# Kernel tuning notes

Measured on AMD Instinct MI355X. Metric: run time of the kernel, lower is better.

## Reference

```python
import jax, jax.numpy as jnp
import numpy as np

NUM_CAPS = 8
IN_CH = 768
OUT_CH = 64  # == num_routes
BATCH = 16384


def setup_inputs() -> dict:
    key = jax.random.key(0)
    ks = jax.random.split(key, 9)
    lim = 1.0 / np.sqrt(IN_CH)  # torch Linear default init range
    inp = {
        'img_emb': jax.random.normal(ks[0], (BATCH, IN_CH), jnp.float32),
        'capt_emb': jax.random.normal(ks[1], (BATCH, IN_CH), jnp.float32),
        'dct_emb': jax.random.normal(ks[2], (BATCH, IN_CH), jnp.float32),
        'W_img': jax.random.uniform(ks[3], (NUM_CAPS, OUT_CH, IN_CH), jnp.float32, -lim, lim),
        'b_img': jax.random.uniform(ks[4], (NUM_CAPS, OUT_CH), jnp.float32, -lim, lim),
        'W_capt': jax.random.uniform(ks[5], (NUM_CAPS, OUT_CH, IN_CH), jnp.float32, -lim, lim),
        'b_capt': jax.random.uniform(ks[6], (NUM_CAPS, OUT_CH), jnp.float32, -lim, lim),
        'W_dct': jax.random.uniform(ks[7], (NUM_CAPS, OUT_CH, IN_CH), jnp.float32, -lim, lim),
        'b_dct': jax.random.uniform(ks[8], (NUM_CAPS, OUT_CH), jnp.float32, -lim, lim),
    }
    return inp


def _project(x, W, b):
    # x: [B, I]; W: [C, R, I]; b: [C, R] -> [B, R, C]
    # torch: per-capsule Linear y = x @ W_c.T + b_c, viewed [B, R, 1], cat on last dim
    y = jnp.einsum('bi,cri->brc', x, W) + b.T[None]  # [B, R, C]
    return y


def _squash(u, epsilon=1e-07):
    sq = jnp.sum(u * u, axis=-1, keepdims=True)  # [B, 3R, 1]
    safe_norm = jnp.sqrt(sq + epsilon)
    return sq * u / ((1.0 + sq) * safe_norm)


def reference(img_emb, capt_emb, dct_emb, W_img, b_img, W_capt, b_capt, W_dct, b_dct):
    u_img = _project(img_emb, W_img, b_img)      # [B, 64, 8]
    u_capt = _project(capt_emb, W_capt, b_capt)  # [B, 64, 8]
    u_dct = _project(dct_emb, W_dct, b_dct)      # [B, 64, 8]
    combined = jnp.concatenate([u_img, u_capt, u_dct], axis=1)  # [B, 192, 8]
    return _squash(combined)
```

## Files before the change

### kernel.cpp

```cpp
#include <hip/hip_runtime.h>

typedef __attribute__((ext_vector_type(8))) short short8;
typedef __attribute__((ext_vector_type(4))) float floatx4;
typedef __attribute__((ext_vector_type(4))) unsigned int uintx4;

#if __has_builtin(__builtin_amdgcn_cvt_pk_bf16_f32)
typedef __attribute__((ext_vector_type(2))) __bf16 bf16x2;
__device__ __forceinline__ unsigned int pk_bf16(float a, float b) {
  bf16x2 v = __builtin_amdgcn_cvt_pk_bf16_f32(a, b);
  return __builtin_bit_cast(unsigned int, v);
}
#else
__device__ __forceinline__ unsigned int bf16_1(float f) {
  unsigned int u = __builtin_bit_cast(unsigned int, f);
  return (u + 0x7fffu + ((u >> 16) & 1u)) >> 16;
}
__device__ __forceinline__ unsigned int pk_bf16(float a, float b) {
  return bf16_1(a) | (bf16_1(b) << 16);
}
#endif


__global__ __launch_bounds__(256) void prep_w(
    const float* __restrict__ Wi, const float* __restrict__ Wc, const float* __restrict__ Wd,
    const float* __restrict__ bi, const float* __restrict__ bc, const float* __restrict__ bd,
    uintx4* __restrict__ Bprep, float* __restrict__ biasPrep) {
  const int t = blockIdx.x * 256 + threadIdx.x;
  const int l = t & 63;
  const int frag = t >> 6;
  const int nt = frag & 3;
  const int q = frag >> 2;
  const int ks = q % 24;
  const int q2 = q / 24;
  const int h = q2 & 7;
  const int mod = q2 >> 3;
  const int n16 = h * 4 + nt;
  const float* __restrict__ W = (mod == 0) ? Wi : ((mod == 1) ? Wc : Wd);

  const int n = n16 * 16 + (l & 15);
  const int r = n >> 3;
  const int c = n & 7;
  const int i0 = ks * 32 + (l >> 4) * 8;
  const float* src = W + (size_t)(c * 64 + r) * 768 + i0;
  floatx4 f0 = *(const floatx4*)(src);
  floatx4 f1 = *(const floatx4*)(src + 4);
  uintx4 p;
  p.x = pk_bf16(f0.x, f0.y);
  p.y = pk_bf16(f0.z, f0.w);
  p.z = pk_bf16(f1.x, f1.y);
  p.w = pk_bf16(f1.z, f1.w);
  Bprep[(size_t)frag * 64 + l] = p;

  if (t < 1536) {
    const int m2 = t >> 9;
    const int nn = t & 511;
    const float* bb = (m2 == 0) ? bi : ((m2 == 1) ? bc : bd);
    biasPrep[t] = bb[(nn & 7) * 64 + (nn >> 3)];
  }
}

#define LOADA(aa, kk)                                                        \
  {                                                                          \
    _Pragma("unroll") for (int mt = 0; mt < 2; ++mt)                         \
        aa[mt] = Afr[((kk) * 2 + mt) * 64 +                                  \
                     ((ln ^ (((kk) * 4 + quad) & 15)) + (quad << 4))];       \
  }

#define LOADB(bb, kk)                                                        \
  {                                                                          \
    _Pragma("unroll") for (int n2 = 0; n2 < 4; ++n2)                         \
        bb[n2] = bbase[((kk) * 4 + n2) * 64];                                \
  }

#define COMP(aa, bb)                                                     \
  {                                                                      \
    _Pragma("unroll") for (int mt = 0; mt < 2; ++mt)                     \
    {                                                                    \
      short8 af = __builtin_bit_cast(short8, aa[mt]);                    \
      _Pragma("unroll") for (int n2 = 0; n2 < 4; ++n2)                   \
          acc[mt][n2] = __builtin_amdgcn_mfma_f32_16x16x32_bf16(         \
              af, __builtin_bit_cast(short8, bb[n2]), acc[mt][n2], 0, 0, \
              0);                                                        \
    }                                                                    \
  }

__global__ __launch_bounds__(512, 4) void caps_fused(
    const float* __restrict__ x0, const float* __restrict__ x1, const float* __restrict__ x2,
    const uintx4* __restrict__ Bprep, const float* __restrict__ biasPrep,
    float* __restrict__ out) {
  __shared__ unsigned long long As64[48 * 128];

  const int tid = threadIdx.x;
  const int bx0 = blockIdx.x;
  const int bx = (bx0 & 7) * 192 + (bx0 >> 3);
  const int mod = bx >> 9;
  const int bm = bx & 511;
  const float* __restrict__ X = (mod == 0) ? x0 : ((mod == 1) ? x1 : x2);

  const float* src = X + (size_t)bm * 32 * 768;
#pragma unroll
  for (int i = 0; i < 12; ++i) {
    const int idx = i * 2048 + tid * 4;
    floatx4 f = __builtin_nontemporal_load((const floatx4*)(src + idx));
    const int m = (unsigned)idx / 768u;
    const int k = idx - m * 768;
    const int ks = k >> 5;
    const int kk = k & 31;
    const int qk = kk >> 3;
    const int jh = (kk >> 2) & 1;
    const int mt = m >> 4;
    const int lnn = m & 15;
    const int p = (ks * 4 + qk) & 15;
    const int slot = (lnn ^ p) + (qk << 4);
    unsigned long long w =
        ((unsigned long long)pk_bf16(f.z, f.w) << 32) | pk_bf16(f.x, f.y);
    As64[(((ks * 2 + mt) * 64 + slot) << 1) + jh] = w;
  }
  __syncthreads();

  const int lane = tid & 63;
  const int ln = lane & 15;
  const int quad = lane >> 4;
  const int wv = tid >> 6;

  const uintx4* Afr = (const uintx4*)As64;
  const uintx4* bbase = Bprep + (size_t)(mod * 8 + wv) * (96 * 64) + lane;

  floatx4 acc[2][4] = {};
  uintx4 a0[2], a1[2], a2[2], b0[4], b1[4], b2[4];

  LOADA(a0, 0); LOADB(b0, 0);
  LOADA(a1, 1); LOADB(b1, 1);
  LOADA(a2, 2); LOADB(b2, 2);
#pragma unroll
  for (int it = 0; it < 7; ++it) {
    const int s = 3 * it;
    COMP(a0, b0);
    LOADA(a0, s + 3); LOADB(b0, s + 3);
    COMP(a1, b1);
    LOADA(a1, s + 4); LOADB(b1, s + 4);
    COMP(a2, b2);
    LOADA(a2, s + 5); LOADB(b2, s + 5);
  }
  COMP(a0, b0);
  COMP(a1, b1);
  COMP(a2, b2);

  const int col0 = mod * 512 + wv * 64 + ln;
  float bias[4];
#pragma unroll
  for (int n2 = 0; n2 < 4; ++n2) bias[n2] = biasPrep[col0 + n2 * 16];

#pragma unroll
  for (int mt = 0; mt < 2; ++mt) {
    float* opm = out + (size_t)(bm * 32 + mt * 16 + quad * 4) * 1536 + col0;
#pragma unroll
    for (int jj = 0; jj < 4; ++jj) {
      float* opj = opm + jj * 1536;
#pragma unroll
      for (int n2 = 0; n2 < 4; ++n2) {
        float u = acc[mt][n2][jj] + bias[n2];
        float s = u * u;
        s += __shfl_xor(s, 1);
        s += __shfl_xor(s, 2);
        s += __shfl_xor(s, 4);
#if __has_builtin(__builtin_amdgcn_rsqf) && __has_builtin(__builtin_amdgcn_rcpf)
        float sc = s * __builtin_amdgcn_rsqf(s + 1e-7f) *
                   __builtin_amdgcn_rcpf(1.0f + s);
#else
        float sc = s / ((1.0f + s) * sqrtf(s + 1e-7f));
#endif
        opj[n2 * 16] = u * sc;
      }
    }
  }
}

extern "C" void kernel_launch(void* const* d_in, const int* in_sizes, int n_in,
                              void* d_out, int out_size, void* d_ws, size_t ws_size,
                              hipStream_t stream) {
  const float* ximg = (const float*)d_in[0];
  const float* xcapt = (const float*)d_in[1];
  const float* xdct = (const float*)d_in[2];
  const float* Wi = (const float*)d_in[3];
  const float* bi = (const float*)d_in[4];
  const float* Wc = (const float*)d_in[5];
  const float* bc = (const float*)d_in[6];
  const float* Wd = (const float*)d_in[7];
  const float* bd = (const float*)d_in[8];

  uintx4* Bprep = (uintx4*)d_ws;
  float* biasPrep = (float*)((char*)d_ws + 2304 * 1024);

  hipLaunchKernelGGL(prep_w, dim3(576), dim3(256), 0, stream,
                     Wi, Wc, Wd, bi, bc, bd, Bprep, biasPrep);
  hipLaunchKernelGGL(caps_fused, dim3(1536), dim3(512), 0, stream,
                     ximg, xcapt, xdct, (const uintx4*)Bprep, biasPrep,
                     (float*)d_out);
}
```

Before: 92.79 us.

## Make caps kernel persistent with register-resident weight fragments per half-strip

The fused kernel becomes persistent with 510 blocks. Each block handles one modality and one half of the 512 output columns and loops over row tiles with a stride of 85. Each wave loads its 48 bf16 B fragments into registers once, so the per-tile weight reloads from global or L2 go away. The cost is that every A tile is now staged and converted twice, once per column half. The design also needs heavy register use (launch bounds drop to 2 blocks), loses the nontemporal loads, and has no overlap between the A-tile load and compute within a block.

```diff
diff --git a/kernel.cpp b/kernel.cpp
--- a/kernel.cpp
+++ b/kernel.cpp
@@ -66,111 +66,117 @@
                      ((ln ^ (((kk) * 4 + quad) & 15)) + (quad << 4))];       \
   }
 
-#define LOADB(bb, kk)                                                        \
-  {                                                                          \
-    _Pragma("unroll") for (int n2 = 0; n2 < 4; ++n2)                         \
-        bb[n2] = bbase[((kk) * 4 + n2) * 64];                                \
-  }
-
-#define COMP(aa, bb)                                                     \
+#define COMP(aa, kk)                                                     \
   {                                                                      \
     _Pragma("unroll") for (int mt = 0; mt < 2; ++mt)                     \
     {                                                                    \
       short8 af = __builtin_bit_cast(short8, aa[mt]);                    \
-      _Pragma("unroll") for (int n2 = 0; n2 < 4; ++n2)                   \
+      _Pragma("unroll") for (int n2 = 0; n2 < 2; ++n2)                   \
           acc[mt][n2] = __builtin_amdgcn_mfma_f32_16x16x32_bf16(         \
-              af, __builtin_bit_cast(short8, bb[n2]), acc[mt][n2], 0, 0, \
-              0);                                                        \
+              af, __builtin_bit_cast(short8, Bfr[(kk) * 2 + n2]),        \
+              acc[mt][n2], 0, 0, 0);                                     \
     }                                                                    \
   }
 
-__global__ __launch_bounds__(512, 4) void caps_fused(
+__global__ __launch_bounds__(512, 2) void caps_fused(
     const float* __restrict__ x0, const float* __restrict__ x1, const float* __restrict__ x2,
     const uintx4* __restrict__ Bprep, const float* __restrict__ biasPrep,
     float* __restrict__ out) {
   __shared__ unsigned long long As64[48 * 128];
 
   const int tid = threadIdx.x;
-  const int bx0 = blockIdx.x;
-  const int bx = (bx0 & 7) * 192 + (bx0 >> 3);
-  const int mod = bx >> 9;
-  const int bm = bx & 511;
+  const int bxx = blockIdx.x;
+  const int strip = bxx % 6;
+  const int idx = bxx / 6;
+  const int mod = strip >> 1;
+  const int half = strip & 1;
   const float* __restrict__ X = (mod == 0) ? x0 : ((mod == 1) ? x1 : x2);
-
-  const float* src = X + (size_t)bm * 32 * 768;
-#pragma unroll
-  for (int i = 0; i < 12; ++i) {
-    const int idx = i * 2048 + tid * 4;
-    floatx4 f = __builtin_nontemporal_load((const floatx4*)(src + idx));
-    const int m = (unsigned)idx / 768u;
-    const int k = idx - m * 768;
-    const int ks = k >> 5;
-    const int kk = k & 31;
-    const int qk = kk >> 3;
-    const int jh = (kk >> 2) & 1;
-    const int mt = m >> 4;
-    const int lnn = m & 15;
-    const int p = (ks * 4 + qk) & 15;
-    const int slot = (lnn ^ p) + (qk << 4);
-    unsigned long long w =
-        ((unsigned long long)pk_bf16(f.z, f.w) << 32) | pk_bf16(f.x, f.y);
-    As64[(((ks * 2 + mt) * 64 + slot) << 1) + jh] = w;
-  }
-  __syncthreads();
 
   const int lane = tid & 63;
   const int ln = lane & 15;
   const int quad = lane >> 4;
   const int wv = tid >> 6;
 
+  const uintx4* bbase =
+      Bprep +
+      (size_t)((mod * 8 + half * 4 + (wv >> 1)) * 96 + (wv & 1) * 2) * 64 +
+      lane;
+  uintx4 Bfr[48];
+#pragma unroll
+  for (int ks = 0; ks < 24; ++ks)
+#pragma unroll
+    for (int n2 = 0; n2 < 2; ++n2)
+      Bfr[ks * 2 + n2] = bbase[(ks * 4 + n2) * 64];
+
+  const int col0 = mod * 512 + half * 256 + wv * 32 + ln;
+  const float bias0 = biasPrep[col0];
+  const float bias1 = biasPrep[col0 + 16];
+
   const uintx4* Afr = (const uintx4*)As64;
-  const uintx4* bbase = Bprep + (size_t)(mod * 8 + wv) * (96 * 64) + lane;
-
-  floatx4 acc[2][4] = {};
-  uintx4 a0[2], a1[2], a2[2], b0[4], b1[4], b2[4];
-
-  LOADA(a0, 0); LOADB(b0, 0);
-  LOADA(a1, 1); LOADB(b1, 1);
-  LOADA(a2, 2); LOADB(b2, 2);
-#pragma unroll
-  for (int it = 0; it < 7; ++it) {
-    const int s = 3 * it;
-    COMP(a0, b0);
-    LOADA(a0, s + 3); LOADB(b0, s + 3);
-    COMP(a1, b1);
-    LOADA(a1, s + 4); LOADB(b1, s + 4);
-    COMP(a2, b2);
-    LOADA(a2, s + 5); LOADB(b2, s + 5);
-  }
-  COMP(a0, b0);
-  COMP(a1, b1);
-  COMP(a2, b2);
-
-  const int col0 = mod * 512 + wv * 64 + ln;
-  float bias[4];
-#pragma unroll
-  for (int n2 = 0; n2 < 4; ++n2) bias[n2] = biasPrep[col0 + n2 * 16];
-
-#pragma unroll
-  for (int mt = 0; mt < 2; ++mt) {
-    float* opm = out + (size_t)(bm * 32 + mt * 16 + quad * 4) * 1536 + col0;
-#pragma unroll
-    for (int jj = 0; jj < 4; ++jj) {
-      float* opj = opm + jj * 1536;
-#pragma unroll
-      for (int n2 = 0; n2 < 4; ++n2) {
-        float u = acc[mt][n2][jj] + bias[n2];
-        float s = u * u;
-        s += __shfl_xor(s, 1);
-        s += __shfl_xor(s, 2);
-        s += __shfl_xor(s, 4);
+
+#pragma unroll 1
+  for (int rt = idx; rt < 512; rt += 85) {
+    if (rt != idx) __syncthreads();
+
+    const float* src = X + (size_t)rt * 32 * 768;
+#pragma unroll
+    for (int i = 0; i < 12; ++i) {
+      const int fidx = i * 2048 + tid * 4;
+      floatx4 f = *(const floatx4*)(src + fidx);
+      const int m = (unsigned)fidx / 768u;
+      const int k = fidx - m * 768;
+      const int ks = k >> 5;
+      const int kk = k & 31;
+      const int qk = kk >> 3;
+      const int jh = (kk >> 2) & 1;
+      const int mt = m >> 4;
+      const int lnn = m & 15;
+      const int p = (ks * 4 + qk) & 15;
+      const int slot = (lnn ^ p) + (qk << 4);
+      unsigned long long w =
+          ((unsigned long long)pk_bf16(f.z, f.w) << 32) | pk_bf16(f.x, f.y);
+      As64[(((ks * 2 + mt) * 64 + slot) << 1) + jh] = w;
+    }
+    __syncthreads();
+
+    floatx4 acc[2][2];
+#pragma unroll
+    for (int mt = 0; mt < 2; ++mt)
+#pragma unroll
+      for (int n2 = 0; n2 < 2; ++n2) acc[mt][n2] = (floatx4)(0.0f);
+
+    uintx4 a0[2], a1[2], a2[2];
+    LOADA(a0, 0); LOADA(a1, 1); LOADA(a2, 2);
+#pragma unroll
+    for (int it = 0; it < 7; ++it) {
+      const int s = 3 * it;
+      COMP(a0, s);     LOADA(a0, s + 3);
+      COMP(a1, s + 1); LOADA(a1, s + 4);
+      COMP(a2, s + 2); LOADA(a2, s + 5);
+    }
+    COMP(a0, 21); COMP(a1, 22); COMP(a2, 23);
+
+#pragma unroll
+    for (int mt = 0; mt < 2; ++mt) {
+      float* opm = out + (size_t)(rt * 32 + mt * 16 + quad * 4) * 1536 + col0;
+#pragma unroll
+      for (int jj = 0; jj < 4; ++jj) {
+        float* opj = opm + jj * 1536;
+#pragma unroll
+        for (int n2 = 0; n2 < 2; ++n2) {
+          float u = acc[mt][n2][jj] + (n2 ? bias1 : bias0);
+          float s = u * u;
+          s += __shfl_xor(s, 1);
+          s += __shfl_xor(s, 2);
+          s += __shfl_xor(s, 4);
 #if __has_builtin(__builtin_amdgcn_rsqf) && __has_builtin(__builtin_amdgcn_rcpf)
-        float sc = s * __builtin_amdgcn_rsqf(s + 1e-7f) *
-                   __builtin_amdgcn_rcpf(1.0f + s);
+          float sc = s * __builtin_amdgcn_rsqf(s + 1e-7f) *
+                     __builtin_amdgcn_rcpf(1.0f + s);
 #else
-        float sc = s / ((1.0f + s) * sqrtf(s + 1e-7f));
+          float sc = s / ((1.0f + s) * sqrtf(s + 1e-7f));
 #endif
-        opj[n2 * 16] = u * sc;
+          opj[n2 * 16] = u * sc;
+        }
       }
     }
   }
@@ -194,7 +200,7 @@
 
   hipLaunchKernelGGL(prep_w, dim3(576), dim3(256), 0, stream,
                      Wi, Wc, Wd, bi, bc, bd, Bprep, biasPrep);
-  hipLaunchKernelGGL(caps_fused, dim3(1536), dim3(512), 0, stream,
+  hipLaunchKernelGGL(caps_fused, dim3(510), dim3(512), 0, stream,
                      ximg, xcapt, xdct, (const uintx4*)Bprep, biasPrep,
                      (float*)d_out);
 }
```

Measured after the change: 96.35 us. 3.8% more time.
